# Performance work log

Hardware: AMD Instinct MI355X
Metric: run time of the kernel (lower is better)

Reference implementation:

```python
import jax, jax.numpy as jnp
import numpy as np

N, E, F_IN, HID, H, NC, G = 50000, 800000, 128, 64, 4, 64, 128
EPS_BN = 1e-5


def setup_inputs() -> dict:
    key = jax.random.key(0)
    ks = jax.random.split(key, 32)
    inp = {}
    inp['x'] = jax.random.normal(ks[0], (N, F_IN), dtype=jnp.float32)
    inp['edge_index'] = jax.random.randint(ks[1], (2, E), 0, N, dtype=jnp.int32)
    inp['batch'] = jnp.sort(jax.random.randint(ks[2], (N,), 0, G, dtype=jnp.int32))
    dims = [(F_IN, HID, H, True), (HID * H, HID, H, True), (HID * H, NC, 1, False)]
    k = 3
    for li, (fin, c, h, concat) in enumerate(dims):
        out_flat = c * h if concat else c
        inp[f'W{li}'] = jax.random.normal(ks[k], (fin, h * c), dtype=jnp.float32) * (1.0 / np.sqrt(fin)); k += 1
        inp[f'asrc{li}'] = jax.random.normal(ks[k], (h, c), dtype=jnp.float32) * 0.1; k += 1
        inp[f'adst{li}'] = jax.random.normal(ks[k], (h, c), dtype=jnp.float32) * 0.1; k += 1
        inp[f'b{li}'] = jnp.zeros((out_flat,), dtype=jnp.float32)
        inp[f'gamma{li}'] = jnp.ones((out_flat,), dtype=jnp.float32)
        inp[f'beta{li}'] = jnp.zeros((out_flat,), dtype=jnp.float32)
    return inp


def gat_layer(x, src, dst, W, asrc, adst, b, heads, out_ch, concat):
    n = x.shape[0]
    h = (x @ W).reshape(n, heads, out_ch)                      # [N,H,C]
    a_s = jnp.sum(h * asrc, axis=-1)                           # [N,H]
    a_d = jnp.sum(h * adst, axis=-1)                           # [N,H]
    e = jax.nn.leaky_relu(a_s[src] + a_d[dst], 0.2)            # [E',H]
    m = jax.ops.segment_max(e, dst, num_segments=n)            # per-target max
    e = jnp.exp(e - m[dst])
    s = jax.ops.segment_sum(e, dst, num_segments=n)
    alpha = e / (s[dst] + 1e-16)                               # softmax over in-edges
    msg = alpha[:, :, None] * h[src]                           # [E',H,C]
    out = jax.ops.segment_sum(msg, dst, num_segments=n)        # [N,H,C]
    out = out.reshape(n, heads * out_ch) if concat else out.mean(axis=1)
    return out + b


def batchnorm(x, gamma, beta):
    mu = x.mean(axis=0)
    var = x.var(axis=0)  # biased, as torch BN training-mode
    return (x - mu) * jax.lax.rsqrt(var + EPS_BN) * gamma + beta


def reference(x, edge_index, batch, W0, asrc0, adst0, b0, gamma0, beta0,
              W1, asrc1, adst1, b1, gamma1, beta1,
              W2, asrc2, adst2, b2, gamma2, beta2):
    n = x.shape[0]
    loop = jnp.arange(n, dtype=edge_index.dtype)
    src = jnp.concatenate([edge_index[0], loop])  # add self loops (PyG default)
    dst = jnp.concatenate([edge_index[1], loop])
    layers = [(W0, asrc0, adst0, b0, gamma0, beta0, H, HID, True),
              (W1, asrc1, adst1, b1, gamma1, beta1, H, HID, True),
              (W2, asrc2, adst2, b2, gamma2, beta2, 1, NC, False)]
    xs = []
    for (W, asrc, adst, b, gamma, beta, heads, oc, concat) in layers:
        x = jax.nn.elu(gat_layer(x, src, dst, W, asrc, adst, b, heads, oc, concat))
        x = batchnorm(x, gamma, beta)
        xs.append(x)
    x_pool = jnp.concatenate([jax.ops.segment_sum(xx, batch, num_segments=G) for xx in xs], axis=1)
    return (x_pool, jnp.concatenate(xs, axis=1))
```

## Files before the change

kernel.cpp:

```cpp
#include <hip/hip_runtime.h>
#include <math.h>

#define N_NODES 50000
#define NUM_E   800000
#define E_TOT   (NUM_E + N_NODES)
#define M_PAD   50048
#define NGRAPH  128
#define XS_COLS 576
#define EPS_BN  1e-5f

static inline int ceil_div(int a, int b) { return (a + b - 1) / b; }

typedef __attribute__((ext_vector_type(8))) short short8;
typedef __attribute__((ext_vector_type(4))) float f32x4;

__device__ __forceinline__ float bf2f(ushort u) {
    union { unsigned int i; float f; } v; v.i = ((unsigned int)u) << 16; return v.f;
}
__device__ __forceinline__ ushort f2bf(float f) {
    union { float f; unsigned int i; } v; v.f = f;
    unsigned int r = v.i + 0x7FFF + ((v.i >> 16) & 1);
    return (ushort)(r >> 16);
}
__device__ __forceinline__ float lrelu(float l) { return l > 0.f ? l : 0.2f * l; }

__global__ __launch_bounds__(256)
void prep_w(const float* __restrict__ W0, const float* __restrict__ W1,
            const float* __restrict__ W2,
            ushort* __restrict__ Wt0, ushort* __restrict__ Wt1, ushort* __restrict__ Wt2)
{
    int j = blockIdx.x * 256 + threadIdx.x;
    if (j < 256 * 128) { Wt0[j] = f2bf(W0[(size_t)(j % 128) * 256 + (j / 128)]); return; }
    j -= 256 * 128;
    if (j < 256 * 256) { Wt1[j] = f2bf(W1[(size_t)(j % 256) * 256 + (j / 256)]); return; }
    j -= 256 * 256;
    if (j < 64 * 256)  { Wt2[j] = f2bf(W2[(size_t)(j % 256) * 64 + (j / 256)]); }
}

template<bool AF32>
__global__ __launch_bounds__(512)
void gemm_bf16_w(const void* __restrict__ Av, int lda,
                 const ushort* __restrict__ Bt, int ldb,
                 ushort* __restrict__ C, int M, int K,
                 const float* __restrict__ asrc, const float* __restrict__ adst,
                 float* __restrict__ a_s, float* __restrict__ a_d)
{
    __shared__ __align__(16) ushort As[128][64 + 8];
    __shared__ __align__(16) ushort Bs[256][64 + 8];
    const int tid = threadIdx.x;
    const int lane = tid & 63;
    const int w = tid >> 6;
    const int m0 = blockIdx.x * 128;

    f32x4 acc[16] = {};

    for (int k0 = 0; k0 < K; k0 += 64) {
#pragma unroll
        for (int j = 0; j < 2; ++j) {
            int c = tid + j * 512;
            int r = c >> 3, cc = (c & 7) * 8;
            if constexpr (AF32) {
                const float* Af = (const float*)Av;
                int m = m0 + r; if (m >= M) m = M - 1;
                float4 v0 = *reinterpret_cast<const float4*>(Af + (size_t)m * lda + k0 + cc);
                float4 v1 = *reinterpret_cast<const float4*>(Af + (size_t)m * lda + k0 + cc + 4);
                short8 v = {(short)f2bf(v0.x), (short)f2bf(v0.y), (short)f2bf(v0.z), (short)f2bf(v0.w),
                            (short)f2bf(v1.x), (short)f2bf(v1.y), (short)f2bf(v1.z), (short)f2bf(v1.w)};
                *reinterpret_cast<short8*>(&As[r][cc]) = v;
            } else {
                const ushort* Ab = (const ushort*)Av;
                short8 v = *reinterpret_cast<const short8*>(Ab + (size_t)(m0 + r) * lda + k0 + cc);
                *reinterpret_cast<short8*>(&As[r][cc]) = v;
            }
        }
#pragma unroll
        for (int j = 0; j < 4; ++j) {
            int c = tid + j * 512;
            int r = c >> 3, cc = (c & 7) * 8;
            short8 v = *reinterpret_cast<const short8*>(Bt + (size_t)r * ldb + k0 + cc);
            *reinterpret_cast<short8*>(&Bs[r][cc]) = v;
        }
        __syncthreads();
#pragma unroll
        for (int kc = 0; kc < 64; kc += 32) {
            short8 a = *reinterpret_cast<const short8*>(&As[w * 16 + (lane & 15)][kc + (lane >> 4) * 8]);
#pragma unroll
            for (int nf = 0; nf < 16; ++nf) {
                short8 b = *reinterpret_cast<const short8*>(&Bs[nf * 16 + (lane & 15)][kc + (lane >> 4) * 8]);
                acc[nf] = __builtin_amdgcn_mfma_f32_16x16x32_bf16(a, b, acc[nf], 0, 0, 0);
            }
        }
        __syncthreads();
    }

    const int mbase = m0 + w * 16 + (lane >> 4) * 4;
#pragma unroll
    for (int r = 0; r < 4; ++r) {
        int m = mbase + r;
        if (m < M) {
#pragma unroll
            for (int nf = 0; nf < 16; ++nf)
                C[(size_t)m * 256 + nf * 16 + (lane & 15)] = f2bf(acc[nf][r]);
        }
    }

    float asl[16], adl[16];
#pragma unroll
    for (int nf = 0; nf < 16; ++nf) {
        int col = nf * 16 + (lane & 15);
        asl[nf] = asrc[col];
        adl[nf] = adst[col];
    }
#pragma unroll
    for (int r = 0; r < 4; ++r) {
        float ps[4] = {0.f, 0.f, 0.f, 0.f};
        float pd[4] = {0.f, 0.f, 0.f, 0.f};
#pragma unroll
        for (int nf = 0; nf < 16; ++nf) {
            int h = nf >> 2;
            ps[h] = fmaf(acc[nf][r], asl[nf], ps[h]);
            pd[h] = fmaf(acc[nf][r], adl[nf], pd[h]);
        }
#pragma unroll
        for (int h = 0; h < 4; ++h) {
#pragma unroll
            for (int o = 1; o < 16; o <<= 1) {
                ps[h] += __shfl_xor(ps[h], o, 64);
                pd[h] += __shfl_xor(pd[h], o, 64);
            }
        }
        int m = mbase + r;
        if ((lane & 15) == 0 && m < M) {
#pragma unroll
            for (int h = 0; h < 4; ++h) {
                a_s[(size_t)m * 4 + h] = ps[h];
                a_d[(size_t)m * 4 + h] = pd[h];
            }
        }
    }
}

template<int BM, int BN, int BK, int H>
__global__ __launch_bounds__(256)
void gemm_bf16(const ushort* __restrict__ A, int lda,
               const ushort* __restrict__ Bt, int ldb,
               ushort* __restrict__ C, int ldc, int M, int K,
               const float* __restrict__ asrc, const float* __restrict__ adst,
               float* __restrict__ a_s, float* __restrict__ a_d)
{
    static_assert(BM == 128 && BN == 64 && BK == 64, "tuned variant");
    __shared__ __align__(16) ushort As[BM][BK + 8];
    __shared__ __align__(16) ushort Bs[BN][BK + 8];
    const int tid = threadIdx.x;
    const int lane = tid & 63;
    const int w = tid >> 6;
    const int m0 = blockIdx.x * BM;
    const int n0 = blockIdx.y * BN;

    f32x4 acc[2][4] = {};

    for (int k0 = 0; k0 < K; k0 += BK) {
#pragma unroll
        for (int j = 0; j < 4; ++j) {
            int c = tid + j * 256;
            int r = c >> 3, cc = (c & 7) * 8;
            short8 v = *reinterpret_cast<const short8*>(A + (size_t)(m0 + r) * lda + k0 + cc);
            *reinterpret_cast<short8*>(&As[r][cc]) = v;
        }
#pragma unroll
        for (int j = 0; j < 2; ++j) {
            int c = tid + j * 256;
            int r = c >> 3, cc = (c & 7) * 8;
            short8 v = *reinterpret_cast<const short8*>(Bt + (size_t)(n0 + r) * ldb + k0 + cc);
            *reinterpret_cast<short8*>(&Bs[r][cc]) = v;
        }
        __syncthreads();
#pragma unroll
        for (int kc = 0; kc < BK; kc += 32) {
            short8 a[2], b[4];
#pragma unroll
            for (int mf = 0; mf < 2; ++mf)
                a[mf] = *reinterpret_cast<const short8*>(&As[w * 32 + mf * 16 + (lane & 15)][kc + (lane >> 4) * 8]);
#pragma unroll
            for (int nf = 0; nf < 4; ++nf)
                b[nf] = *reinterpret_cast<const short8*>(&Bs[nf * 16 + (lane & 15)][kc + (lane >> 4) * 8]);
#pragma unroll
            for (int mf = 0; mf < 2; ++mf)
#pragma unroll
                for (int nf = 0; nf < 4; ++nf)
                    acc[mf][nf] = __builtin_amdgcn_mfma_f32_16x16x32_bf16(a[mf], b[nf], acc[mf][nf], 0, 0, 0);
        }
        __syncthreads();
    }

#pragma unroll
    for (int mf = 0; mf < 2; ++mf) {
        int mbase = m0 + w * 32 + mf * 16 + (lane >> 4) * 4;
#pragma unroll
        for (int r = 0; r < 4; ++r) {
            int m = mbase + r;
            if (m < M) {
#pragma unroll
                for (int nf = 0; nf < 4; ++nf)
                    C[(size_t)m * ldc + n0 + nf * 16 + (lane & 15)] = f2bf(acc[mf][nf][r]);
            }
        }
    }

    const int hd = blockIdx.y;
    float asl[4], adl[4];
#pragma unroll
    for (int nf = 0; nf < 4; ++nf) {
        int col = n0 + nf * 16 + (lane & 15);
        asl[nf] = asrc[col];
        adl[nf] = adst[col];
    }
#pragma unroll
    for (int mf = 0; mf < 2; ++mf) {
#pragma unroll
        for (int r = 0; r < 4; ++r) {
            float ps = 0.f, pd = 0.f;
#pragma unroll
            for (int nf = 0; nf < 4; ++nf) {
                ps = fmaf(acc[mf][nf][r], asl[nf], ps);
                pd = fmaf(acc[mf][nf][r], adl[nf], pd);
            }
#pragma unroll
            for (int o = 1; o < 16; o <<= 1) {
                ps += __shfl_xor(ps, o, 64);
                pd += __shfl_xor(pd, o, 64);
            }
            int m = m0 + w * 32 + mf * 16 + (lane >> 4) * 4 + r;
            if ((lane & 15) == 0 && m < M) {
                a_s[(size_t)m * H + hd] = ps;
                a_d[(size_t)m * H + hd] = pd;
            }
        }
    }
}

template<int H, int C>
__global__ __launch_bounds__(256)
void gat_fused2(const int* __restrict__ offs, const int* __restrict__ ssrc,
                const float* __restrict__ a_s, const float* __restrict__ a_d,
                const ushort* __restrict__ hf, const float* __restrict__ bias,
                ushort* __restrict__ ybuf, float* __restrict__ bnsum)
{
    constexpr int V = (H * C) / 32;
    constexpr int OF = H * C;
    __shared__ float alsh[4][2][64 * H];
    __shared__ int   ssh[4][2][64];
    __shared__ float ysh[8][OF];
    const int tid = threadIdx.x;
    const int lane = tid & 63;
    const int wv = tid >> 6;
    const int half = lane >> 5;
    const int ll = lane & 31;
    const int dl = wv * 2 + half;
    const int dst = blockIdx.x * 8 + dl;
    const int e0 = offs[dst], e1 = offs[dst + 1];
    const int deg = e1 - e0;
    const int hd = (ll * V) / C;

    float ad[H];
    if constexpr (H == 4) {
        float4 v = *reinterpret_cast<const float4*>(a_d + (size_t)dst * 4);
        ad[0] = v.x; ad[1] = v.y; ad[2] = v.z; ad[3] = v.w;
    } else ad[0] = a_d[dst];

    float acc[V];
#pragma unroll
    for (int k = 0; k < V; ++k) acc[k] = 0.f;

    if (deg <= 64) {
        const bool a0 = ll < deg;
        const bool a1 = 32 + ll < deg;
        const int s0 = ssrc[e0 + (a0 ? ll : 0)];
        const int s1 = ssrc[e0 + (a1 ? 32 + ll : 0)];
        float l0[H], l1[H], mx[H], sm[H];
        if constexpr (H == 4) {
            float4 v0 = *reinterpret_cast<const float4*>(a_s + (size_t)s0 * 4);
            float4 v1 = *reinterpret_cast<const float4*>(a_s + (size_t)s1 * 4);
            l0[0] = lrelu(v0.x + ad[0]); l0[1] = lrelu(v0.y + ad[1]);
            l0[2] = lrelu(v0.z + ad[2]); l0[3] = lrelu(v0.w + ad[3]);
            l1[0] = lrelu(v1.x + ad[0]); l1[1] = lrelu(v1.y + ad[1]);
            l1[2] = lrelu(v1.z + ad[2]); l1[3] = lrelu(v1.w + ad[3]);
        } else {
            l0[0] = lrelu(a_s[s0] + ad[0]);
            l1[0] = lrelu(a_s[s1] + ad[0]);
        }
#pragma unroll
        for (int t = 0; t < H; ++t) {
            float m = a0 ? l0[t] : -INFINITY;
            if (a1) m = fmaxf(m, l1[t]);
#pragma unroll
            for (int o = 1; o < 32; o <<= 1) m = fmaxf(m, __shfl_xor(m, o, 64));
            mx[t] = m;
            float s = (a0 ? __expf(l0[t] - m) : 0.f) + (a1 ? __expf(l1[t] - m) : 0.f);
#pragma unroll
            for (int o = 1; o < 32; o <<= 1) s += __shfl_xor(s, o, 64);
            sm[t] = s;
        }
        float inv[H];
#pragma unroll
        for (int t = 0; t < H; ++t) inv[t] = 1.f / (sm[t] + 1e-16f);
        if (a0) {
            ssh[wv][half][ll] = s0;
            if constexpr (H == 4) {
                float4 av = {__expf(l0[0] - mx[0]) * inv[0], __expf(l0[1] - mx[1]) * inv[1],
                             __expf(l0[2] - mx[2]) * inv[2], __expf(l0[3] - mx[3]) * inv[3]};
                *reinterpret_cast<float4*>(&alsh[wv][half][ll * 4]) = av;
            } else alsh[wv][half][ll] = __expf(l0[0] - mx[0]) * inv[0];
        }
        if (a1) {
            ssh[wv][half][32 + ll] = s1;
            if constexpr (H == 4) {
                float4 av = {__expf(l1[0] - mx[0]) * inv[0], __expf(l1[1] - mx[1]) * inv[1],
                             __expf(l1[2] - mx[2]) * inv[2], __expf(l1[3] - mx[3]) * inv[3]};
                *reinterpret_cast<float4*>(&alsh[wv][half][(32 + ll) * 4]) = av;
            } else alsh[wv][half][32 + ll] = __expf(l1[0] - mx[0]) * inv[0];
        }

        const ushort* hlane = hf + (size_t)ll * V;
        int j = 0;
        for (; j + 3 < deg; j += 4) {
            int sj[4]; float al[4];
#pragma unroll
            for (int k = 0; k < 4; ++k) {
                sj[k] = ssh[wv][half][j + k];
                al[k] = alsh[wv][half][(j + k) * H + hd];
            }
            if constexpr (V == 8) {
                short8 hv[4];
#pragma unroll
                for (int k = 0; k < 4; ++k)
                    hv[k] = *reinterpret_cast<const short8*>(hlane + (size_t)sj[k] * OF);
#pragma unroll
                for (int k = 0; k < 4; ++k)
#pragma unroll
                    for (int i = 0; i < 8; ++i)
                        acc[i] = fmaf(al[k], bf2f((ushort)hv[k][i]), acc[i]);
            } else {
                ushort2 hv[4];
#pragma unroll
                for (int k = 0; k < 4; ++k)
                    hv[k] = *reinterpret_cast<const ushort2*>(hlane + (size_t)sj[k] * OF);
#pragma unroll
                for (int k = 0; k < 4; ++k) {
                    acc[0] = fmaf(al[k], bf2f(hv[k].x), acc[0]);
                    acc[1] = fmaf(al[k], bf2f(hv[k].y), acc[1]);
                }
            }
        }
        for (; j < deg; ++j) {
            int sj = ssh[wv][half][j];
            float al = alsh[wv][half][j * H + hd];
            if constexpr (V == 8) {
                short8 hv = *reinterpret_cast<const short8*>(hlane + (size_t)sj * OF);
#pragma unroll
                for (int i = 0; i < 8; ++i)
                    acc[i] = fmaf(al, bf2f((ushort)hv[i]), acc[i]);
            } else {
                ushort2 hv = *reinterpret_cast<const ushort2*>(hlane + (size_t)sj * OF);
                acc[0] = fmaf(al, bf2f(hv.x), acc[0]);
                acc[1] = fmaf(al, bf2f(hv.y), acc[1]);
            }
        }
    } else {
        float mx[H], sm[H];
#pragma unroll
        for (int t = 0; t < H; ++t) mx[t] = -INFINITY;
        for (int e = e0 + ll; e < e1; e += 32) {
            int s = ssrc[e];
            float asv[H];
            if constexpr (H == 4) {
                float4 v = *reinterpret_cast<const float4*>(a_s + (size_t)s * 4);
                asv[0] = v.x; asv[1] = v.y; asv[2] = v.z; asv[3] = v.w;
            } else asv[0] = a_s[s];
#pragma unroll
            for (int t = 0; t < H; ++t) mx[t] = fmaxf(mx[t], lrelu(asv[t] + ad[t]));
        }
#pragma unroll
        for (int t = 0; t < H; ++t)
#pragma unroll
            for (int o = 1; o < 32; o <<= 1) mx[t] = fmaxf(mx[t], __shfl_xor(mx[t], o, 64));
#pragma unroll
        for (int t = 0; t < H; ++t) sm[t] = 0.f;
        for (int e = e0 + ll; e < e1; e += 32) {
            int s = ssrc[e];
            float asv[H];
            if constexpr (H == 4) {
                float4 v = *reinterpret_cast<const float4*>(a_s + (size_t)s * 4);
                asv[0] = v.x; asv[1] = v.y; asv[2] = v.z; asv[3] = v.w;
            } else asv[0] = a_s[s];
#pragma unroll
            for (int t = 0; t < H; ++t) sm[t] += __expf(lrelu(asv[t] + ad[t]) - mx[t]);
        }
#pragma unroll
        for (int t = 0; t < H; ++t)
#pragma unroll
            for (int o = 1; o < 32; o <<= 1) sm[t] += __shfl_xor(sm[t], o, 64);

        float mxl = mx[0], sml = sm[0], adl = ad[0];
#pragma unroll
        for (int t = 1; t < H; ++t) {
            mxl = (hd == t) ? mx[t] : mxl;
            sml = (hd == t) ? sm[t] : sml;
            adl = (hd == t) ? ad[t] : adl;
        }
        const float invl = 1.f / (sml + 1e-16f);
        const ushort* hlane = hf + (size_t)ll * V;
        for (int e = e0; e < e1; ++e) {
            int s0 = ssrc[e];
            float al0 = __expf(lrelu(a_s[(size_t)s0 * H + hd] + adl) - mxl) * invl;
            if constexpr (V == 8) {
                short8 hv = *reinterpret_cast<const short8*>(hlane + (size_t)s0 * OF);
#pragma unroll
                for (int i = 0; i < 8; ++i)
                    acc[i] = fmaf(al0, bf2f((ushort)hv[i]), acc[i]);
            } else {
                ushort2 hv = *reinterpret_cast<const ushort2*>(hlane + (size_t)s0 * OF);
                acc[0] = fmaf(al0, bf2f(hv.x), acc[0]);
                acc[1] = fmaf(al0, bf2f(hv.y), acc[1]);
            }
        }
    }

    float res[V];
#pragma unroll
    for (int i = 0; i < V; ++i) {
        float t = acc[i] + bias[ll * V + i];
        res[i] = t > 0.f ? t : (expf(t) - 1.f);
    }
    if constexpr (V == 8) {
        short8 yv = {(short)f2bf(res[0]), (short)f2bf(res[1]), (short)f2bf(res[2]), (short)f2bf(res[3]),
                     (short)f2bf(res[4]), (short)f2bf(res[5]), (short)f2bf(res[6]), (short)f2bf(res[7])};
        *reinterpret_cast<short8*>(&ybuf[(size_t)dst * OF + ll * 8]) = yv;
        *reinterpret_cast<f32x4*>(&ysh[dl][ll * 8 + 0]) = f32x4{res[0], res[1], res[2], res[3]};
        *reinterpret_cast<f32x4*>(&ysh[dl][ll * 8 + 4]) = f32x4{res[4], res[5], res[6], res[7]};
    } else {
        ushort2 yv = {f2bf(res[0]), f2bf(res[1])};
        *reinterpret_cast<ushort2*>(&ybuf[(size_t)dst * OF + ll * 2]) = yv;
        ysh[dl][ll * 2 + 0] = res[0];
        ysh[dl][ll * 2 + 1] = res[1];
    }
    __syncthreads();
    if (tid < OF) {
        float s = 0.f, s2 = 0.f;
#pragma unroll
        for (int d = 0; d < 8; ++d) {
            float v = ysh[d][tid];
            s += v;
            s2 = fmaf(v, v, s2);
        }
        int slot = blockIdx.x & 7;
        atomicAdd(&bnsum[(size_t)slot * 2 * OF + tid], s);
        atomicAdd(&bnsum[(size_t)slot * 2 * OF + OF + tid], s2);
    }
}

__global__ void edge_count(const int* __restrict__ ei, int* __restrict__ counts)
{
    int i = blockIdx.x * blockDim.x + threadIdx.x;
    if (i >= E_TOT) return;
    int dst = (i < NUM_E) ? ei[NUM_E + i] : (i - NUM_E);
    atomicAdd(&counts[dst], 1);
}

__global__ void edge_scatter(const int* __restrict__ ei, int* __restrict__ cursor,
                             int* __restrict__ ssrc)
{
    int i = blockIdx.x * blockDim.x + threadIdx.x;
    if (i >= E_TOT) return;
    int src, dst;
    if (i < NUM_E) { src = ei[i]; dst = ei[NUM_E + i]; }
    else           { src = dst = i - NUM_E; }
    int pos = atomicAdd(&cursor[dst], 1);
    ssrc[pos] = src;
}

__global__ void scan_block(const int* __restrict__ in, int n,
                           int* __restrict__ incl, int* __restrict__ bsum)
{
    __shared__ int sh[256];
    int tid = threadIdx.x;
    int i = blockIdx.x * 256 + tid;
    int v = (i < n) ? in[i] : 0;
    sh[tid] = v;
    __syncthreads();
    for (int o = 1; o < 256; o <<= 1) {
        int t = (tid >= o) ? sh[tid - o] : 0;
        __syncthreads();
        sh[tid] += t;
        __syncthreads();
    }
    if (i < n) incl[i] = sh[tid];
    if (tid == 255) bsum[blockIdx.x] = sh[255];
}

__global__ void scan_final(const int* __restrict__ incl, const int* __restrict__ in,
                           const int* __restrict__ bsum, int n,
                           int* __restrict__ offs, int* __restrict__ cursor)
{
    __shared__ int sh[256];
    const int tid = threadIdx.x;
    const int bi = blockIdx.x;
    sh[tid] = (tid < bi) ? bsum[tid] : 0;
    __syncthreads();
    for (int o = 128; o > 0; o >>= 1) {
        if (tid < o) sh[tid] += sh[tid + o];
        __syncthreads();
    }
    const int pref = sh[0];
    int i = bi * 256 + tid;
    if (i >= n) return;
    int excl = incl[i] - in[i] + pref;
    offs[i] = excl;
    cursor[i] = excl;
    if (i == n - 1) offs[n] = incl[i] + pref;
}

template<int OF>
__global__ void bn_finalize(const float* __restrict__ bnsum, const float* __restrict__ gamma,
                            const float* __restrict__ beta, float* __restrict__ ss)
{
    int c = threadIdx.x;
    if (c >= OF) return;
    float s = 0.f, s2 = 0.f;
#pragma unroll
    for (int slot = 0; slot < 8; ++slot) {
        s += bnsum[(size_t)slot * 2 * OF + c];
        s2 += bnsum[(size_t)slot * 2 * OF + OF + c];
    }
    float mean = s / (float)N_NODES;
    float var = s2 / (float)N_NODES - mean * mean;
    float inv = rsqrtf(var + EPS_BN);
    float sc = inv * gamma[c];
    ss[c] = sc;
    ss[OF + c] = beta[c] - mean * sc;
}

template<int OF, bool WB>
__global__ __launch_bounds__(256)
void bn_apply_pool(const ushort* __restrict__ y, float* __restrict__ xs, int ldx,
                   const float* __restrict__ ss, ushort* __restrict__ xb, int ldxb,
                   const int* __restrict__ batch, float* __restrict__ pool, int poff)
{
    const int tid = threadIdx.x;
    constexpr int CP = OF / 2;
    constexpr int RS = 256 / CP;
    const int c = (tid % CP) * 2;
    const int rsub = tid / CP;
    const int r0 = blockIdx.x * 16;
    const float sc0 = ss[c], sh0 = ss[OF + c];
    const float sc1 = ss[c + 1], sh1 = ss[OF + c + 1];
    float ps0 = 0.f, ps1 = 0.f;
    int curg = batch[r0 + rsub];
#pragma unroll
    for (int i = 0; i < 16 / RS; ++i) {
        int r = r0 + rsub + i * RS;
        int g = batch[r];
        if (g != curg) {
            atomicAdd(&pool[(size_t)curg * XS_COLS + poff + c], ps0);
            atomicAdd(&pool[(size_t)curg * XS_COLS + poff + c + 1], ps1);
            ps0 = ps1 = 0.f; curg = g;
        }
        ushort2 hv = *reinterpret_cast<const ushort2*>(y + (size_t)r * OF + c);
        float v0 = fmaf(bf2f(hv.x), sc0, sh0);
        float v1 = fmaf(bf2f(hv.y), sc1, sh1);
        float2 vv = {v0, v1};
        *reinterpret_cast<float2*>(&xs[(size_t)r * ldx + c]) = vv;
        if constexpr (WB) {
            ushort2 bb = {f2bf(v0), f2bf(v1)};
            *reinterpret_cast<ushort2*>(&xb[(size_t)r * ldxb + c]) = bb;
        }
        ps0 += v0; ps1 += v1;
    }
    atomicAdd(&pool[(size_t)curg * XS_COLS + poff + c], ps0);
    atomicAdd(&pool[(size_t)curg * XS_COLS + poff + c + 1], ps1);
}

extern "C" void kernel_launch(void* const* d_in, const int* in_sizes, int n_in,
                              void* d_out, int out_size, void* d_ws, size_t ws_size,
                              hipStream_t stream)
{
    const float* x     = (const float*)d_in[0];
    const int*   ei    = (const int*)d_in[1];
    const int*   batch = (const int*)d_in[2];
    const float* W[3]    = {(const float*)d_in[3],  (const float*)d_in[9],  (const float*)d_in[15]};
    const float* asrc[3] = {(const float*)d_in[4],  (const float*)d_in[10], (const float*)d_in[16]};
    const float* adst[3] = {(const float*)d_in[5],  (const float*)d_in[11], (const float*)d_in[17]};
    const float* bia[3]  = {(const float*)d_in[6],  (const float*)d_in[12], (const float*)d_in[18]};
    const float* gam[3]  = {(const float*)d_in[7],  (const float*)d_in[13], (const float*)d_in[19]};
    const float* bet[3]  = {(const float*)d_in[8],  (const float*)d_in[14], (const float*)d_in[20]};

    char* wp = (char*)d_ws;
    auto alloc = [&](size_t bytes) -> void* {
        void* p = (void*)wp;
        wp += (bytes + 255) & ~(size_t)255;
        return p;
    };
    ushort* hbf   = (ushort*)alloc((size_t)N_NODES * 256 * 2);
    ushort* ybuf  = (ushort*)alloc((size_t)N_NODES * 256 * 2);
    ushort* AbfA  = (ushort*)alloc((size_t)M_PAD * 256 * 2);
    float*  a_s   = (float*)alloc((size_t)N_NODES * 4 * 4);
    float*  a_d   = (float*)alloc((size_t)N_NODES * 4 * 4);
    int*    counts = (int*)alloc((size_t)N_NODES * 4);
    int*    offs   = (int*)alloc((size_t)(N_NODES + 1) * 4);
    int*    cursor = (int*)alloc((size_t)N_NODES * 4);
    int*    incl   = (int*)alloc((size_t)N_NODES * 4);
    int*    bsums  = (int*)alloc(1024);
    int*    ssrc   = (int*)alloc((size_t)E_TOT * 4);
    float*  bnsum  = (float*)alloc((size_t)8 * 2 * 256 * 4);
    float*  bnss   = (float*)alloc(2 * 256 * 4);
    ushort* Wt0    = (ushort*)alloc(256 * 128 * 2);
    ushort* Wt1    = (ushort*)alloc(256 * 256 * 2);
    ushort* Wt2    = (ushort*)alloc(64 * 256 * 2);

    float* pool = (float*)d_out;
    float* xs   = pool + (size_t)NGRAPH * XS_COLS;

    hipMemsetAsync(counts, 0, (size_t)N_NODES * 4, stream);
    hipMemsetAsync(pool, 0, (size_t)NGRAPH * XS_COLS * 4, stream);
    edge_count<<<ceil_div(E_TOT, 256), 256, 0, stream>>>(ei, counts);
    const int NSB = ceil_div(N_NODES, 256);
    scan_block<<<NSB, 256, 0, stream>>>(counts, N_NODES, incl, bsums);
    scan_final<<<NSB, 256, 0, stream>>>(incl, counts, bsums, N_NODES, offs, cursor);
    edge_scatter<<<ceil_div(E_TOT, 256), 256, 0, stream>>>(ei, cursor, ssrc);
    const int PREP_ITEMS = 256 * 128 + 256 * 256 + 64 * 256;
    prep_w<<<ceil_div(PREP_ITEMS, 256), 256, 0, stream>>>(W[0], W[1], W[2], Wt0, Wt1, Wt2);

    const int NW2 = ceil_div(N_NODES, 8);
    const int NMB = ceil_div(N_NODES, 128);
    const int NBA = N_NODES / 16;

    {
        gemm_bf16_w<true><<<NMB, 512, 0, stream>>>(x, 128, Wt0, 128, hbf, N_NODES, 128,
                                                   asrc[0], adst[0], a_s, a_d);
        hipMemsetAsync(bnsum, 0, (size_t)8 * 2 * 256 * 4, stream);
        gat_fused2<4, 64><<<NW2, 256, 0, stream>>>(offs, ssrc, a_s, a_d, hbf, bia[0], ybuf, bnsum);
        bn_finalize<256><<<1, 256, 0, stream>>>(bnsum, gam[0], bet[0], bnss);
        bn_apply_pool<256, true><<<NBA, 256, 0, stream>>>(ybuf, xs + 0, XS_COLS, bnss, AbfA, 256,
                                                          batch, pool, 0);
    }
    {
        gemm_bf16_w<false><<<NMB, 512, 0, stream>>>(AbfA, 256, Wt1, 256, hbf, N_NODES, 256,
                                                    asrc[1], adst[1], a_s, a_d);
        hipMemsetAsync(bnsum, 0, (size_t)8 * 2 * 256 * 4, stream);
        gat_fused2<4, 64><<<NW2, 256, 0, stream>>>(offs, ssrc, a_s, a_d, hbf, bia[1], ybuf, bnsum);
        bn_finalize<256><<<1, 256, 0, stream>>>(bnsum, gam[1], bet[1], bnss);
        bn_apply_pool<256, true><<<NBA, 256, 0, stream>>>(ybuf, xs + 256, XS_COLS, bnss, AbfA, 256,
                                                          batch, pool, 256);
    }
    {
        dim3 grid(NMB, 1);
        gemm_bf16<128, 64, 64, 1><<<grid, 256, 0, stream>>>(AbfA, 256, Wt2, 256, hbf, 64, N_NODES, 256,
                                                            asrc[2], adst[2], a_s, a_d);
        hipMemsetAsync(bnsum, 0, (size_t)8 * 2 * 256 * 4, stream);
        gat_fused2<1, 64><<<NW2, 256, 0, stream>>>(offs, ssrc, a_s, a_d, hbf, bia[2], ybuf, bnsum);
        bn_finalize<64><<<1, 64, 0, stream>>>(bnsum, gam[2], bet[2], bnss);
        bn_apply_pool<64, false><<<NBA, 256, 0, stream>>>(ybuf, xs + 512, XS_COLS, bnss, nullptr, 0,
                                                          batch, pool, 512);
    }
}
```

Measured before the change: 461.7 us.

## Fuse BN apply into next-layer GEMM A-load, drop bf16 activation copy

The next layer's GEMM now reads the raw bf16 GAT output and applies the batchnorm scale and shift while staging the A tile into shared memory. The bf16 normalized copy written by bn_apply_pool is removed, along with its buffer. The per-layer bnsum memsets are replaced by one up-front memset, with bn_finalize zeroing the sums after it reads them. bn_apply_pool is also widened to 4 columns per thread, trading a full N×256 bf16 write and read plus extra launches for some extra ALU work in the GEMM load path.

```diff
diff --git a/kernel.cpp b/kernel.cpp
--- a/kernel.cpp
+++ b/kernel.cpp
@@ -37,9 +37,10 @@
     if (j < 64 * 256)  { Wt2[j] = f2bf(W2[(size_t)(j % 256) * 64 + (j / 256)]); }
 }
 
-template<bool AF32>
+template<int AMODE>
 __global__ __launch_bounds__(512)
 void gemm_bf16_w(const void* __restrict__ Av, int lda,
+                 const float* __restrict__ bnsc, const float* __restrict__ bnsh,
                  const ushort* __restrict__ Bt, int ldb,
                  ushort* __restrict__ C, int M, int K,
                  const float* __restrict__ asrc, const float* __restrict__ adst,
@@ -59,7 +60,7 @@
         for (int j = 0; j < 2; ++j) {
             int c = tid + j * 512;
             int r = c >> 3, cc = (c & 7) * 8;
-            if constexpr (AF32) {
+            if constexpr (AMODE == 0) {
                 const float* Af = (const float*)Av;
                 int m = m0 + r; if (m >= M) m = M - 1;
                 float4 v0 = *reinterpret_cast<const float4*>(Af + (size_t)m * lda + k0 + cc);
@@ -69,7 +70,20 @@
                 *reinterpret_cast<short8*>(&As[r][cc]) = v;
             } else {
                 const ushort* Ab = (const ushort*)Av;
-                short8 v = *reinterpret_cast<const short8*>(Ab + (size_t)(m0 + r) * lda + k0 + cc);
+                short8 y = *reinterpret_cast<const short8*>(Ab + (size_t)(m0 + r) * lda + k0 + cc);
+                float4 sa = *reinterpret_cast<const float4*>(&bnsc[k0 + cc]);
+                float4 sb = *reinterpret_cast<const float4*>(&bnsc[k0 + cc + 4]);
+                float4 ha = *reinterpret_cast<const float4*>(&bnsh[k0 + cc]);
+                float4 hb = *reinterpret_cast<const float4*>(&bnsh[k0 + cc + 4]);
+                short8 v;
+                v[0] = (short)f2bf(fmaf(bf2f((ushort)y[0]), sa.x, ha.x));
+                v[1] = (short)f2bf(fmaf(bf2f((ushort)y[1]), sa.y, ha.y));
+                v[2] = (short)f2bf(fmaf(bf2f((ushort)y[2]), sa.z, ha.z));
+                v[3] = (short)f2bf(fmaf(bf2f((ushort)y[3]), sa.w, ha.w));
+                v[4] = (short)f2bf(fmaf(bf2f((ushort)y[4]), sb.x, hb.x));
+                v[5] = (short)f2bf(fmaf(bf2f((ushort)y[5]), sb.y, hb.y));
+                v[6] = (short)f2bf(fmaf(bf2f((ushort)y[6]), sb.z, hb.z));
+                v[7] = (short)f2bf(fmaf(bf2f((ushort)y[7]), sb.w, hb.w));
                 *reinterpret_cast<short8*>(&As[r][cc]) = v;
             }
         }
@@ -140,22 +154,22 @@
     }
 }
 
-template<int BM, int BN, int BK, int H>
 __global__ __launch_bounds__(256)
-void gemm_bf16(const ushort* __restrict__ A, int lda,
-               const ushort* __restrict__ Bt, int ldb,
-               ushort* __restrict__ C, int ldc, int M, int K,
-               const float* __restrict__ asrc, const float* __restrict__ adst,
-               float* __restrict__ a_s, float* __restrict__ a_d)
-{
-    static_assert(BM == 128 && BN == 64 && BK == 64, "tuned variant");
+void gemm_bf16_n(const ushort* __restrict__ A, int lda,
+                 const float* __restrict__ bnsc, const float* __restrict__ bnsh,
+                 const ushort* __restrict__ Bt, int ldb,
+                 ushort* __restrict__ C, int ldc, int M, int K,
+                 const float* __restrict__ asrc, const float* __restrict__ adst,
+                 float* __restrict__ a_s, float* __restrict__ a_d)
+{
+    constexpr int BM = 128, BN = 64, BK = 64;
     __shared__ __align__(16) ushort As[BM][BK + 8];
     __shared__ __align__(16) ushort Bs[BN][BK + 8];
     const int tid = threadIdx.x;
     const int lane = tid & 63;
     const int w = tid >> 6;
     const int m0 = blockIdx.x * BM;
-    const int n0 = blockIdx.y * BN;
+    const int n0 = 0;
 
     f32x4 acc[2][4] = {};
 
@@ -164,7 +178,20 @@
         for (int j = 0; j < 4; ++j) {
             int c = tid + j * 256;
             int r = c >> 3, cc = (c & 7) * 8;
-            short8 v = *reinterpret_cast<const short8*>(A + (size_t)(m0 + r) * lda + k0 + cc);
+            short8 y = *reinterpret_cast<const short8*>(A + (size_t)(m0 + r) * lda + k0 + cc);
+            float4 sa = *reinterpret_cast<const float4*>(&bnsc[k0 + cc]);
+            float4 sb = *reinterpret_cast<const float4*>(&bnsc[k0 + cc + 4]);
+            float4 ha = *reinterpret_cast<const float4*>(&bnsh[k0 + cc]);
+            float4 hb = *reinterpret_cast<const float4*>(&bnsh[k0 + cc + 4]);
+            short8 v;
+            v[0] = (short)f2bf(fmaf(bf2f((ushort)y[0]), sa.x, ha.x));
+            v[1] = (short)f2bf(fmaf(bf2f((ushort)y[1]), sa.y, ha.y));
+            v[2] = (short)f2bf(fmaf(bf2f((ushort)y[2]), sa.z, ha.z));
+            v[3] = (short)f2bf(fmaf(bf2f((ushort)y[3]), sa.w, ha.w));
+            v[4] = (short)f2bf(fmaf(bf2f((ushort)y[4]), sb.x, hb.x));
+            v[5] = (short)f2bf(fmaf(bf2f((ushort)y[5]), sb.y, hb.y));
+            v[6] = (short)f2bf(fmaf(bf2f((ushort)y[6]), sb.z, hb.z));
+            v[7] = (short)f2bf(fmaf(bf2f((ushort)y[7]), sb.w, hb.w));
             *reinterpret_cast<short8*>(&As[r][cc]) = v;
         }
 #pragma unroll
@@ -207,7 +234,6 @@
         }
     }
 
-    const int hd = blockIdx.y;
     float asl[4], adl[4];
 #pragma unroll
     for (int nf = 0; nf < 4; ++nf) {
@@ -232,8 +258,8 @@
             }
             int m = m0 + w * 32 + mf * 16 + (lane >> 4) * 4 + r;
             if ((lane & 15) == 0 && m < M) {
-                a_s[(size_t)m * H + hd] = ps;
-                a_d[(size_t)m * H + hd] = pd;
+                a_s[(size_t)m] = ps;
+                a_d[(size_t)m] = pd;
             }
         }
     }
@@ -521,7 +547,7 @@
 }
 
 template<int OF>
-__global__ void bn_finalize(const float* __restrict__ bnsum, const float* __restrict__ gamma,
+__global__ void bn_finalize(float* __restrict__ bnsum, const float* __restrict__ gamma,
                             const float* __restrict__ beta, float* __restrict__ ss)
 {
     int c = threadIdx.x;
@@ -531,6 +557,8 @@
     for (int slot = 0; slot < 8; ++slot) {
         s += bnsum[(size_t)slot * 2 * OF + c];
         s2 += bnsum[(size_t)slot * 2 * OF + OF + c];
+        bnsum[(size_t)slot * 2 * OF + c] = 0.f;
+        bnsum[(size_t)slot * 2 * OF + OF + c] = 0.f;
     }
     float mean = s / (float)N_NODES;
     float var = s2 / (float)N_NODES - mean * mean;
@@ -540,44 +568,46 @@
     ss[OF + c] = beta[c] - mean * sc;
 }
 
-template<int OF, bool WB>
+template<int OF>
 __global__ __launch_bounds__(256)
 void bn_apply_pool(const ushort* __restrict__ y, float* __restrict__ xs, int ldx,
-                   const float* __restrict__ ss, ushort* __restrict__ xb, int ldxb,
+                   const float* __restrict__ ss,
                    const int* __restrict__ batch, float* __restrict__ pool, int poff)
 {
+    constexpr int CG = OF / 4;
+    constexpr int RS = 256 / CG;
     const int tid = threadIdx.x;
-    constexpr int CP = OF / 2;
-    constexpr int RS = 256 / CP;
-    const int c = (tid % CP) * 2;
-    const int rsub = tid / CP;
+    const int c = (tid % CG) * 4;
+    const int rsub = tid / CG;
     const int r0 = blockIdx.x * 16;
-    const float sc0 = ss[c], sh0 = ss[OF + c];
-    const float sc1 = ss[c + 1], sh1 = ss[OF + c + 1];
-    float ps0 = 0.f, ps1 = 0.f;
+    float4 sc = *reinterpret_cast<const float4*>(&ss[c]);
+    float4 sh = *reinterpret_cast<const float4*>(&ss[OF + c]);
+    float4 ps = {0.f, 0.f, 0.f, 0.f};
     int curg = batch[r0 + rsub];
 #pragma unroll
     for (int i = 0; i < 16 / RS; ++i) {
         int r = r0 + rsub + i * RS;
         int g = batch[r];
         if (g != curg) {
-            atomicAdd(&pool[(size_t)curg * XS_COLS + poff + c], ps0);
-            atomicAdd(&pool[(size_t)curg * XS_COLS + poff + c + 1], ps1);
-            ps0 = ps1 = 0.f; curg = g;
-        }
-        ushort2 hv = *reinterpret_cast<const ushort2*>(y + (size_t)r * OF + c);
-        float v0 = fmaf(bf2f(hv.x), sc0, sh0);
-        float v1 = fmaf(bf2f(hv.y), sc1, sh1);
-        float2 vv = {v0, v1};
-        *reinterpret_cast<float2*>(&xs[(size_t)r * ldx + c]) = vv;
-        if constexpr (WB) {
-            ushort2 bb = {f2bf(v0), f2bf(v1)};
-            *reinterpret_cast<ushort2*>(&xb[(size_t)r * ldxb + c]) = bb;
-        }
-        ps0 += v0; ps1 += v1;
-    }
-    atomicAdd(&pool[(size_t)curg * XS_COLS + poff + c], ps0);
-    atomicAdd(&pool[(size_t)curg * XS_COLS + poff + c + 1], ps1);
+            atomicAdd(&pool[(size_t)curg * XS_COLS + poff + c + 0], ps.x);
+            atomicAdd(&pool[(size_t)curg * XS_COLS + poff + c + 1], ps.y);
+            atomicAdd(&pool[(size_t)curg * XS_COLS + poff + c + 2], ps.z);
+            atomicAdd(&pool[(size_t)curg * XS_COLS + poff + c + 3], ps.w);
+            ps = {0.f, 0.f, 0.f, 0.f}; curg = g;
+        }
+        ushort4 hv = *reinterpret_cast<const ushort4*>(y + (size_t)r * OF + c);
+        float4 v;
+        v.x = fmaf(bf2f(hv.x), sc.x, sh.x);
+        v.y = fmaf(bf2f(hv.y), sc.y, sh.y);
+        v.z = fmaf(bf2f(hv.z), sc.z, sh.z);
+        v.w = fmaf(bf2f(hv.w), sc.w, sh.w);
+        *reinterpret_cast<float4*>(&xs[(size_t)r * ldx + c]) = v;
+        ps.x += v.x; ps.y += v.y; ps.z += v.z; ps.w += v.w;
+    }
+    atomicAdd(&pool[(size_t)curg * XS_COLS + poff + c + 0], ps.x);
+    atomicAdd(&pool[(size_t)curg * XS_COLS + poff + c + 1], ps.y);
+    atomicAdd(&pool[(size_t)curg * XS_COLS + poff + c + 2], ps.z);
+    atomicAdd(&pool[(size_t)curg * XS_COLS + poff + c + 3], ps.w);
 }
 
 extern "C" void kernel_launch(void* const* d_in, const int* in_sizes, int n_in,
@@ -601,8 +631,7 @@
         return p;
     };
     ushort* hbf   = (ushort*)alloc((size_t)N_NODES * 256 * 2);
-    ushort* ybuf  = (ushort*)alloc((size_t)N_NODES * 256 * 2);
-    ushort* AbfA  = (ushort*)alloc((size_t)M_PAD * 256 * 2);
+    ushort* ybuf  = (ushort*)alloc((size_t)M_PAD * 256 * 2);
     float*  a_s   = (float*)alloc((size_t)N_NODES * 4 * 4);
     float*  a_d   = (float*)alloc((size_t)N_NODES * 4 * 4);
     int*    counts = (int*)alloc((size_t)N_NODES * 4);
@@ -622,6 +651,7 @@
 
     hipMemsetAsync(counts, 0, (size_t)N_NODES * 4, stream);
     hipMemsetAsync(pool, 0, (size_t)NGRAPH * XS_COLS * 4, stream);
+    hipMemsetAsync(bnsum, 0, (size_t)8 * 2 * 256 * 4, stream);
     edge_count<<<ceil_div(E_TOT, 256), 256, 0, stream>>>(ei, counts);
     const int NSB = ceil_div(N_NODES, 256);
     scan_block<<<NSB, 256, 0, stream>>>(counts, N_NODES, incl, bsums);
@@ -635,31 +665,24 @@
     const int NBA = N_NODES / 16;
 
     {
-        gemm_bf16_w<true><<<NMB, 512, 0, stream>>>(x, 128, Wt0, 128, hbf, N_NODES, 128,
-                                                   asrc[0], adst[0], a_s, a_d);
-        hipMemsetAsync(bnsum, 0, (size_t)8 * 2 * 256 * 4, stream);
+        gemm_bf16_w<0><<<NMB, 512, 0, stream>>>(x, 128, nullptr, nullptr, Wt0, 128, hbf, N_NODES, 128,
+                                                asrc[0], adst[0], a_s, a_d);
         gat_fused2<4, 64><<<NW2, 256, 0, stream>>>(offs, ssrc, a_s, a_d, hbf, bia[0], ybuf, bnsum);
         bn_finalize<256><<<1, 256, 0, stream>>>(bnsum, gam[0], bet[0], bnss);
-        bn_apply_pool<256, true><<<NBA, 256, 0, stream>>>(ybuf, xs + 0, XS_COLS, bnss, AbfA, 256,
-                                                          batch, pool, 0);
+        bn_apply_pool<256><<<NBA, 256, 0, stream>>>(ybuf, xs + 0, XS_COLS, bnss, batch, pool, 0);
     }
     {
-        gemm_bf16_w<false><<<NMB, 512, 0, stream>>>(AbfA, 256, Wt1, 256, hbf, N_NODES, 256,
-                                                    asrc[1], adst[1], a_s, a_d);
-        hipMemsetAsync(bnsum, 0, (size_t)8 * 2 * 256 * 4, stream);
+        gemm_bf16_w<2><<<NMB, 512, 0, stream>>>(ybuf, 256, bnss, bnss + 256, Wt1, 256, hbf, N_NODES, 256,
+                                                asrc[1], adst[1], a_s, a_d);
         gat_fused2<4, 64><<<NW2, 256, 0, stream>>>(offs, ssrc, a_s, a_d, hbf, bia[1], ybuf, bnsum);
         bn_finalize<256><<<1, 256, 0, stream>>>(bnsum, gam[1], bet[1], bnss);
-        bn_apply_pool<256, true><<<NBA, 256, 0, stream>>>(ybuf, xs + 256, XS_COLS, bnss, AbfA, 256,
-                                                          batch, pool, 256);
+        bn_apply_pool<256><<<NBA, 256, 0, stream>>>(ybuf, xs + 256, XS_COLS, bnss, batch, pool, 256);
     }
     {
-        dim3 grid(NMB, 1);
-        gemm_bf16<128, 64, 64, 1><<<grid, 256, 0, stream>>>(AbfA, 256, Wt2, 256, hbf, 64, N_NODES, 256,
-                                                            asrc[2], adst[2], a_s, a_d);
-        hipMemsetAsync(bnsum, 0, (size_t)8 * 2 * 256 * 4, stream);
+        gemm_bf16_n<<<NMB, 256, 0, stream>>>(ybuf, 256, bnss, bnss + 256, Wt2, 256, hbf, 64, N_NODES, 256,
+                                             asrc[2], adst[2], a_s, a_d);
         gat_fused2<1, 64><<<NW2, 256, 0, stream>>>(offs, ssrc, a_s, a_d, hbf, bia[2], ybuf, bnsum);
         bn_finalize<64><<<1, 64, 0, stream>>>(bnsum, gam[2], bet[2], bnss);
-        bn_apply_pool<64, false><<<NBA, 256, 0, stream>>>(ybuf, xs + 512, XS_COLS, bnss, nullptr, 0,
-                                                          batch, pool, 512);
-    }
-}
+        bn_apply_pool<64><<<NBA, 256, 0, stream>>>(ybuf, xs + 512, XS_COLS, bnss, batch, pool, 512);
+    }
+}
```

After: 699.2 us. +51.4%, slower.
